# Kernel optimization log

Hardware: AMD Instinct MI355X
Metric: run time of the kernel (lower is better)

Reference implementation:

```python
import jax, jax.numpy as jnp
import numpy as np

N = 50000
E = 800000
D_IN = 64
D_OUT = 64
H = 8
R = 8  # num_relations; relation id R is reserved for self-loops
NEG_SLOPE = 0.2
EPS = 1e-10


def setup_inputs() -> dict:
    key = jax.random.key(0)
    ks = jax.random.split(key, 7)
    x = jax.random.normal(ks[0], (N, D_IN), jnp.float32)
    # xavier_uniform-like scale for W_tau, kaiming-like for query
    w_scale = (6.0 / (D_IN + D_OUT)) ** 0.5
    W_tau = jax.random.normal(ks[1], (R + 1, D_OUT, D_IN), jnp.float32) * w_scale
    query = jax.random.normal(ks[2], (R + 1, H, 2 * D_OUT // H), jnp.float32) * 0.1
    node_in = jax.random.randint(ks[3], (E,), 0, N, jnp.int32)
    node_out = jax.random.randint(ks[4], (E,), 0, N, jnp.int32)
    relation = jax.random.randint(ks[5], (E,), 0, R, jnp.int32)
    edge_weight = jax.random.uniform(ks[6], (E,), jnp.float32)
    return {"x": x, "W_tau": W_tau, "query": query, "node_in": node_in,
            "node_out": node_out, "relation": relation, "edge_weight": edge_weight}


def reference(x, W_tau, query, node_in, node_out, relation, edge_weight):
    n_node = x.shape[0]
    rp1, d_out, _ = W_tau.shape  # num_relations + 1
    n_head = query.shape[1]

    # append self-loop edges with relation id = num_relations, weight 1
    self_idx = jnp.arange(n_node, dtype=node_in.dtype)
    ni = jnp.concatenate([node_in, self_idx])            # [M]
    no = jnp.concatenate([node_out, self_idx])           # [M]
    rel = jnp.concatenate([relation, jnp.full((n_node,), rp1 - 1, dtype=relation.dtype)])
    ew = jnp.concatenate([edge_weight, jnp.ones((n_node,), edge_weight.dtype)])[:, None]  # [M,1]

    # per-relation linear transform of all nodes: [R+1, N, D_out]
    hidden = jnp.einsum('rdi,ni->rnd', W_tau, x)

    # gather endpoint features per edge (relation-specific)
    h_in = hidden[rel, ni]    # [M, D_out]
    h_out = hidden[rel, no]   # [M, D_out]
    m = h_in.shape[0]

    # interleaved stack then head split, matching torch stack(dim=-1).view
    key_feat = jnp.stack([h_in, h_out], axis=-1).reshape(m, n_head, -1)  # [M,H,2*D/H]
    w = jnp.einsum('mhd,mhd->mh', query[rel], key_feat)                  # [M,H]
    w = jax.nn.leaky_relu(w, NEG_SLOPE)

    # segment softmax (stabilized by per-node max), normalizer is scatter-MEAN (faithful)
    mx = jax.ops.segment_max(w, no, num_segments=n_node)[no]
    att = jnp.exp(w - mx) * ew                                           # [M,H]
    cnt = jax.ops.segment_sum(jnp.ones((m,), x.dtype), no, num_segments=n_node)  # [N]
    norm = (jax.ops.segment_sum(att, no, num_segments=n_node) / cnt[:, None])[no]
    att = att / (norm + EPS)

    value = h_in.reshape(m, n_head, d_out // n_head)                     # [M,H,D/H]
    msg = (att[..., None] * value).reshape(m, d_out)                     # [M,D_out]

    # aggregate: scatter-mean over destination nodes, then ReLU (combine)
    update = jax.ops.segment_sum(msg, no, num_segments=n_node) / cnt[:, None]
    return jax.nn.relu(update)
```

## Files before the change

### kernel.cpp

```cpp
#include <hip/hip_runtime.h>
#include <math.h>

#define N_NODES 50000
#define N_EDGES 800000
#define DOUT 64
#define NHEAD 8
#define RP1 9
#define NEG_SLOPE 0.2f
#define EPS_F 1e-10f
#define M_TOT (N_EDGES + N_NODES)
#define NW (RP1 * DOUT * DOUT)
#define RNG (N_NODES / 8)
#define EPB 2048
#define CHUNKS ((M_TOT + EPB - 1) / EPB)
#define BUCK 48
#define MBLK ((M_TOT + 255) / 256)
#define FILLB (CHUNKS * 8)
#define K1B ((N_NODES + 63) / 64)
#define K1PAD 784

typedef __attribute__((ext_vector_type(8))) short bf16x8;
typedef __attribute__((ext_vector_type(4))) float f32x4;

__device__ __forceinline__ unsigned short f2bf(float f) {
    unsigned int u = __float_as_uint(f);
    unsigned int r = (u + 0x7FFFu + ((u >> 16) & 1u)) >> 16;
    return (unsigned short)r;
}
__device__ __forceinline__ float bf2f(unsigned short s) {
    return __uint_as_float(((unsigned int)s) << 16);
}

__global__ __launch_bounds__(256) void kprep2(const int* __restrict__ node_in,
                                              const int* __restrict__ relation,
                                              const float* __restrict__ edge_weight,
                                              const float* __restrict__ W,
                                              int2* __restrict__ meta_by_m,
                                              unsigned short* __restrict__ Wb,
                                              int* __restrict__ cursor) {
    int m = blockIdx.x * 256 + threadIdx.x;
    if (m < NW / 4) {
        int i = m * 4;
        float4 v = *(const float4*)(W + i);
        ushort4 o; o.x = f2bf(v.x); o.y = f2bf(v.y); o.z = f2bf(v.z); o.w = f2bf(v.w);
        *(ushort4*)(Wb + i) = o;
    }
    if (m < N_NODES) cursor[m] = 0;
    if (m >= M_TOT) return;
    int ni, rl; float ew;
    if (m < N_EDGES) {
        ni = node_in[m]; rl = relation[m]; ew = edge_weight[m];
    } else {
        ni = m - N_EDGES; rl = RP1 - 1; ew = 1.0f;
    }
    int2 v; v.x = ni | (rl << 16); v.y = __float_as_int(ew);
    meta_by_m[m] = v;
}

__global__ __launch_bounds__(256) void kbig(const float* __restrict__ x,
                                            const unsigned short* __restrict__ Wb,
                                            unsigned short* __restrict__ hiddenb,
                                            const int* __restrict__ node_out,
                                            const int2* __restrict__ meta_by_m,
                                            int* __restrict__ cursor,
                                            int2* __restrict__ bucket) {
    const int t = threadIdx.x;

    if (blockIdx.x >= K1PAD) {
        const int f = blockIdx.x - K1PAD;
        const int r = f & 7;
        const int chunk = f >> 3;
        const int lo = r * RNG;
        const int hi = lo + RNG;
        int m = chunk * EPB + t;
#pragma unroll
        for (int it = 0; it < EPB / 256; it++, m += 256) {
            if (m < M_TOT) {
                int2 v = meta_by_m[m];
                int no = (m < N_EDGES) ? node_out[m] : (m - N_EDGES);
                if (no >= lo && no < hi) {
                    int pos = atomicAdd(&cursor[no], 1);
                    if (pos < BUCK) bucket[(size_t)no * BUCK + pos] = v;
                }
            }
        }
        return;
    }

    const int bx = blockIdx.x;
    if (bx >= K1B) return;
    __shared__ float xs[64 * 68];
    __shared__ unsigned short st[4 * 16 * 72];
    const int wv = t >> 6, lane = t & 63;
    const int quad = lane >> 4, l16 = lane & 15;
    const int base = bx * 64 + wv * 16;

    for (int q = t; q < 64 * 64 / 4; q += 256) {
        int flat = q * 4;
        int row = flat >> 6;
        int col = flat & 63;
        int n = bx * 64 + row;
        float4 v = make_float4(0.f, 0.f, 0.f, 0.f);
        if (n < N_NODES) v = *(const float4*)(x + (size_t)n * 64 + col);
        float* p = &xs[row * 68 + col];
        p[0] = v.x; p[1] = v.y; p[2] = v.z; p[3] = v.w;
    }
    __syncthreads();

    int arowl = wv * 16 + l16;
    bf16x8 a0, a1;
#pragma unroll
    for (int j = 0; j < 8; j++) {
        a0[j] = (short)f2bf(xs[arowl * 68 + quad * 8 + j]);
        a1[j] = (short)f2bf(xs[arowl * 68 + quad * 8 + 32 + j]);
    }

    unsigned short* sw = &st[wv * 16 * 72];

    for (int r = 0; r < RP1; r++) {
        const unsigned short* Wr = Wb + r * 4096;
        f32x4 acc[4];
#pragma unroll
        for (int dt = 0; dt < 4; dt++) {
            const bf16x8 b0 = *(const bf16x8*)(Wr + (dt * 16 + l16) * 64 + quad * 8);
            const bf16x8 b1 = *(const bf16x8*)(Wr + (dt * 16 + l16) * 64 + quad * 8 + 32);
            f32x4 c = {0.f, 0.f, 0.f, 0.f};
            c = __builtin_amdgcn_mfma_f32_16x16x32_bf16(a0, b0, c, 0, 0, 0);
            c = __builtin_amdgcn_mfma_f32_16x16x32_bf16(a1, b1, c, 0, 0, 0);
            acc[dt] = c;
        }
#pragma unroll
        for (int dt = 0; dt < 4; dt++) {
#pragma unroll
            for (int v = 0; v < 4; v++) {
                sw[(quad * 4 + v) * 72 + dt * 16 + l16] = f2bf(acc[dt][v]);
            }
        }
        __threadfence_block();
#pragma unroll
        for (int q = 0; q < 2; q++) {
            int cid = q * 64 + lane;
            int row = cid >> 3;
            int ch = cid & 7;
            int n = base + row;
            if (n < N_NODES) {
                bf16x8 v = *(const bf16x8*)(sw + row * 72 + ch * 8);
                *(bf16x8*)(hiddenb + ((size_t)r * N_NODES + n) * 64 + ch * 8) = v;
            }
        }
        __threadfence_block();
    }
}

__global__ __launch_bounds__(256) void k3_fused2(const unsigned short* __restrict__ hiddenb,
                                                 const float* __restrict__ query,
                                                 const int2* __restrict__ bucket,
                                                 const int* __restrict__ deg,
                                                 float* __restrict__ out) {
    __shared__ float qe[RP1 * 64];
    __shared__ float qo[RP1 * 64];
    __shared__ int2  meta[4][64];
    __shared__ float bho[4][2][72];

    const int t = threadIdx.x;
    for (int q = t; q < RP1 * 64; q += 256) {
        int j = q & 7, rh = q >> 3;
        qe[q] = query[rh * 16 + 2 * j];
        qo[q] = query[rh * 16 + 2 * j + 1];
    }
    __syncthreads();

    const int wv = t >> 6, lane = t & 63;
    const int pairi = blockIdx.x * 4 + wv;
    const int nA = pairi * 2, nB = nA + 1;
    const int e_lo = lane >> 3, h = lane & 7;

    {
        const int prel = lane >> 3, ph = lane & 7;
        bf16x8 ra = *(const bf16x8*)(hiddenb + ((size_t)(prel * N_NODES + nA)) * 64 + ph * 8);
        bf16x8 rb = *(const bf16x8*)(hiddenb + ((size_t)(prel * N_NODES + nB)) * 64 + ph * 8);
        bf16x8 r8 = ra;
        if (lane < 16) {
            int n8 = (lane < 8) ? nA : nB;
            r8 = *(const bf16x8*)(hiddenb + ((size_t)(8 * N_NODES + n8)) * 64 + (lane & 7) * 8);
        }
        const float* qop = &qo[(prel * 8 + ph) * 8];
        float da = 0.f, db = 0.f;
#pragma unroll
        for (int j = 0; j < 8; j++) {
            da += qop[j] * bf2f((unsigned short)ra[j]);
            db += qop[j] * bf2f((unsigned short)rb[j]);
        }
        bho[wv][0][prel * 8 + ph] = da;
        bho[wv][1][prel * 8 + ph] = db;
        if (lane < 16) {
            const float* q8p = &qo[(64 + (lane & 7)) * 8];
            float d8 = 0.f;
#pragma unroll
            for (int j = 0; j < 8; j++) d8 += q8p[j] * bf2f((unsigned short)r8[j]);
            bho[wv][(lane < 8) ? 0 : 1][64 + (lane & 7)] = d8;
        }
    }
    __threadfence_block();

    const int degAi = deg[nA], degBi = deg[nB];
    const int begA = nA * BUCK, endA = begA + min(degAi, BUCK);
    const int begB = nB * BUCK, endB = begB + min(degBi, BUCK);
    const float degA = (float)degAi, degB = (float)degBi;

    float accA[8] = {0.f, 0.f, 0.f, 0.f, 0.f, 0.f, 0.f, 0.f};
    float accB[8] = {0.f, 0.f, 0.f, 0.f, 0.f, 0.f, 0.f, 0.f};
    float spA = 0.f, spB = 0.f;
    int cbA = begA, cbB = begB;

    while (cbA < endA || cbB < endB) {
        const int cA = min(32, endA - cbA);
        const int cB = min(32, endB - cbB);

        int2 mt; mt.x = nA | ((RP1 - 1) << 16); mt.y = 0;
        if (lane < 32) {
            if (lane < cA) mt = bucket[cbA + lane];
        } else {
            int l2 = lane - 32;
            if (l2 < cB) mt = bucket[cbB + l2];
        }
        meta[wv][lane] = mt;
        __threadfence_block();

        const int npA = (cA + 7) >> 3, npB = (cB + 7) >> 3;

        bf16x8 rA[4], rB[4];
        int relA[4], relB[4]; float ewA[4], ewB[4];
#pragma unroll
        for (int p = 0; p < 4; p++) {
            if (p < npA) {
                int2 m2 = meta[wv][p * 8 + e_lo];
                int ni = m2.x & 0xffff, rl = m2.x >> 16;
                relA[p] = rl; ewA[p] = __int_as_float(m2.y);
                rA[p] = *(const bf16x8*)(hiddenb + ((size_t)(rl * N_NODES + ni)) * 64 + h * 8);
            }
            if (p < npB) {
                int2 m2 = meta[wv][32 + p * 8 + e_lo];
                int ni = m2.x & 0xffff, rl = m2.x >> 16;
                relB[p] = rl; ewB[p] = __int_as_float(m2.y);
                rB[p] = *(const bf16x8*)(hiddenb + ((size_t)(rl * N_NODES + ni)) * 64 + h * 8);
            }
        }

#pragma unroll
        for (int p = 0; p < 4; p++) {
            if (p < npA) {
                const float* qp = &qe[(relA[p] * 8 + h) * 8];
                float hif[8];
#pragma unroll
                for (int j = 0; j < 8; j++) hif[j] = bf2f((unsigned short)rA[p][j]);
                float wp = bho[wv][0][relA[p] * 8 + h];
#pragma unroll
                for (int j = 0; j < 8; j++) wp += qp[j] * hif[j];
                wp = (wp > 0.f) ? wp : NEG_SLOPE * wp;
                float pa = __expf(wp) * ewA[p];
#pragma unroll
                for (int j = 0; j < 8; j++) accA[j] += pa * hif[j];
                spA += pa;
            }
            if (p < npB) {
                const float* qp = &qe[(relB[p] * 8 + h) * 8];
                float hif[8];
#pragma unroll
                for (int j = 0; j < 8; j++) hif[j] = bf2f((unsigned short)rB[p][j]);
                float wp = bho[wv][1][relB[p] * 8 + h];
#pragma unroll
                for (int j = 0; j < 8; j++) wp += qp[j] * hif[j];
                wp = (wp > 0.f) ? wp : NEG_SLOPE * wp;
                float pa = __expf(wp) * ewB[p];
#pragma unroll
                for (int j = 0; j < 8; j++) accB[j] += pa * hif[j];
                spB += pa;
            }
        }

        cbA += cA; cbB += cB;
    }

#pragma unroll
    for (int j = 0; j < 8; j++) {
        accA[j] += __shfl_xor(accA[j], 8);
        accA[j] += __shfl_xor(accA[j], 16);
        accA[j] += __shfl_xor(accA[j], 32);
        accB[j] += __shfl_xor(accB[j], 8);
        accB[j] += __shfl_xor(accB[j], 16);
        accB[j] += __shfl_xor(accB[j], 32);
    }
    spA += __shfl_xor(spA, 8); spA += __shfl_xor(spA, 16); spA += __shfl_xor(spA, 32);
    spB += __shfl_xor(spB, 8); spB += __shfl_xor(spB, 16); spB += __shfl_xor(spB, 32);

    if (lane < 8) {
        const float s = 1.f / ((spA / degA + EPS_F) * degA);
        float4 o0, o1;
        o0.x = fmaxf(accA[0] * s, 0.f); o0.y = fmaxf(accA[1] * s, 0.f);
        o0.z = fmaxf(accA[2] * s, 0.f); o0.w = fmaxf(accA[3] * s, 0.f);
        o1.x = fmaxf(accA[4] * s, 0.f); o1.y = fmaxf(accA[5] * s, 0.f);
        o1.z = fmaxf(accA[6] * s, 0.f); o1.w = fmaxf(accA[7] * s, 0.f);
        float* op = out + (size_t)nA * 64 + lane * 8;
        *(float4*)(op) = o0; *(float4*)(op + 4) = o1;
    } else if (lane < 16) {
        const float s = 1.f / ((spB / degB + EPS_F) * degB);
        float4 o0, o1;
        o0.x = fmaxf(accB[0] * s, 0.f); o0.y = fmaxf(accB[1] * s, 0.f);
        o0.z = fmaxf(accB[2] * s, 0.f); o0.w = fmaxf(accB[3] * s, 0.f);
        o1.x = fmaxf(accB[4] * s, 0.f); o1.y = fmaxf(accB[5] * s, 0.f);
        o1.z = fmaxf(accB[6] * s, 0.f); o1.w = fmaxf(accB[7] * s, 0.f);
        float* op = out + (size_t)nB * 64 + (lane - 8) * 8;
        *(float4*)(op) = o0; *(float4*)(op + 4) = o1;
    }
}

extern "C" void kernel_launch(void* const* d_in, const int* in_sizes, int n_in,
                              void* d_out, int out_size, void* d_ws, size_t ws_size,
                              hipStream_t stream) {
    const float* x        = (const float*)d_in[0];
    const float* W_tau    = (const float*)d_in[1];
    const float* query    = (const float*)d_in[2];
    const int*   node_in  = (const int*)d_in[3];
    const int*   node_out = (const int*)d_in[4];
    const int*   relation = (const int*)d_in[5];
    const float* edge_w   = (const float*)d_in[6];
    float* out = (float*)d_out;

    char* ws = (char*)d_ws;
    unsigned short* hiddenb   = (unsigned short*)(ws);
    unsigned short* Wb        = (unsigned short*)(ws + 57600000);
    int2*           meta_by_m = (int2*)(ws + 57673728);
    int2*           bucket    = (int2*)(ws + 64473728);
    int*            cursor    = (int*)(ws + 83673728);

    kprep2<<<MBLK, 256, 0, stream>>>(node_in, relation, edge_w, W_tau,
                                     meta_by_m, Wb, cursor);

    kbig<<<K1PAD + FILLB, 256, 0, stream>>>(x, Wb, hiddenb, node_out, meta_by_m,
                                            cursor, bucket);

    k3_fused2<<<(N_NODES / 2 + 3) / 4, 256, 0, stream>>>(hiddenb, query, bucket,
                                                         cursor, out);
}
```

Before: 178.2 us.

## Load x directly to registers and hoist bucket/hidden loads before query staging

In the transform kernel, the shared-memory staging of x is removed; each lane loads its MFMA A-operand rows straight from global memory, which drops a barrier and the LDS traffic. In the aggregation kernel, the degree, bucket-metadata and self-feature loads are issued before the query table is staged into shared memory, so their latency overlaps that setup. The per-chunk while loop with its shared-memory meta buffer is replaced by a single 32-slot pass that distributes metadata with wave shuffles, plus a separate tail path for nodes with more than 32 edges. The tail path adds code size and some register pressure.

```diff
diff --git a/kernel.cpp b/kernel.cpp
--- a/kernel.cpp
+++ b/kernel.cpp
@@ -89,31 +89,27 @@
 
     const int bx = blockIdx.x;
     if (bx >= K1B) return;
-    __shared__ float xs[64 * 68];
     __shared__ unsigned short st[4 * 16 * 72];
     const int wv = t >> 6, lane = t & 63;
     const int quad = lane >> 4, l16 = lane & 15;
     const int base = bx * 64 + wv * 16;
 
-    for (int q = t; q < 64 * 64 / 4; q += 256) {
-        int flat = q * 4;
-        int row = flat >> 6;
-        int col = flat & 63;
-        int n = bx * 64 + row;
-        float4 v = make_float4(0.f, 0.f, 0.f, 0.f);
-        if (n < N_NODES) v = *(const float4*)(x + (size_t)n * 64 + col);
-        float* p = &xs[row * 68 + col];
-        p[0] = v.x; p[1] = v.y; p[2] = v.z; p[3] = v.w;
-    }
-    __syncthreads();
-
-    int arowl = wv * 16 + l16;
+    int arow = base + l16;
+    if (arow >= N_NODES) arow = N_NODES - 1;
+    const float* xr = x + (size_t)arow * 64 + quad * 8;
+    const float4 f0 = *(const float4*)(xr + 0);
+    const float4 f1 = *(const float4*)(xr + 4);
+    const float4 f2 = *(const float4*)(xr + 32);
+    const float4 f3 = *(const float4*)(xr + 36);
     bf16x8 a0, a1;
-#pragma unroll
-    for (int j = 0; j < 8; j++) {
-        a0[j] = (short)f2bf(xs[arowl * 68 + quad * 8 + j]);
-        a1[j] = (short)f2bf(xs[arowl * 68 + quad * 8 + 32 + j]);
-    }
+    a0[0] = (short)f2bf(f0.x); a0[1] = (short)f2bf(f0.y);
+    a0[2] = (short)f2bf(f0.z); a0[3] = (short)f2bf(f0.w);
+    a0[4] = (short)f2bf(f1.x); a0[5] = (short)f2bf(f1.y);
+    a0[6] = (short)f2bf(f1.z); a0[7] = (short)f2bf(f1.w);
+    a1[0] = (short)f2bf(f2.x); a1[1] = (short)f2bf(f2.y);
+    a1[2] = (short)f2bf(f2.z); a1[3] = (short)f2bf(f2.w);
+    a1[4] = (short)f2bf(f3.x); a1[5] = (short)f2bf(f3.y);
+    a1[6] = (short)f2bf(f3.z); a1[7] = (short)f2bf(f3.w);
 
     unsigned short* sw = &st[wv * 16 * 72];
 
@@ -159,10 +155,28 @@
                                                  float* __restrict__ out) {
     __shared__ float qe[RP1 * 64];
     __shared__ float qo[RP1 * 64];
-    __shared__ int2  meta[4][64];
     __shared__ float bho[4][2][72];
 
     const int t = threadIdx.x;
+    const int wv = t >> 6, lane = t & 63;
+    const int pairi = blockIdx.x * 4 + wv;
+    const int nA = pairi * 2, nB = nA + 1;
+    const int e_lo = lane >> 3, h = lane & 7;
+
+    const int degAi = deg[nA], degBi = deg[nB];
+    const int slot = lane & 31;
+    const int nn = (lane >= 32) ? nB : nA;
+    const int2 mt0 = bucket[(size_t)nn * BUCK + slot];
+
+    const int prel = lane >> 3, ph = lane & 7;
+    const bf16x8 ra = *(const bf16x8*)(hiddenb + ((size_t)(prel * N_NODES + nA)) * 64 + ph * 8);
+    const bf16x8 rb = *(const bf16x8*)(hiddenb + ((size_t)(prel * N_NODES + nB)) * 64 + ph * 8);
+    bf16x8 r8 = ra;
+    if (lane < 16) {
+        int n8 = (lane < 8) ? nA : nB;
+        r8 = *(const bf16x8*)(hiddenb + ((size_t)(8 * N_NODES + n8)) * 64 + (lane & 7) * 8);
+    }
+
     for (int q = t; q < RP1 * 64; q += 256) {
         int j = q & 7, rh = q >> 3;
         qe[q] = query[rh * 16 + 2 * j];
@@ -170,20 +184,7 @@
     }
     __syncthreads();
 
-    const int wv = t >> 6, lane = t & 63;
-    const int pairi = blockIdx.x * 4 + wv;
-    const int nA = pairi * 2, nB = nA + 1;
-    const int e_lo = lane >> 3, h = lane & 7;
-
     {
-        const int prel = lane >> 3, ph = lane & 7;
-        bf16x8 ra = *(const bf16x8*)(hiddenb + ((size_t)(prel * N_NODES + nA)) * 64 + ph * 8);
-        bf16x8 rb = *(const bf16x8*)(hiddenb + ((size_t)(prel * N_NODES + nB)) * 64 + ph * 8);
-        bf16x8 r8 = ra;
-        if (lane < 16) {
-            int n8 = (lane < 8) ? nA : nB;
-            r8 = *(const bf16x8*)(hiddenb + ((size_t)(8 * N_NODES + n8)) * 64 + (lane & 7) * 8);
-        }
         const float* qop = &qo[(prel * 8 + ph) * 8];
         float da = 0.f, db = 0.f;
 #pragma unroll
@@ -203,83 +204,112 @@
     }
     __threadfence_block();
 
-    const int degAi = deg[nA], degBi = deg[nB];
-    const int begA = nA * BUCK, endA = begA + min(degAi, BUCK);
-    const int begB = nB * BUCK, endB = begB + min(degBi, BUCK);
+    const int cA = min(32, degAi);
+    const int cB = min(32, degBi);
+    const int npA = (cA + 7) >> 3, npB = (cB + 7) >> 3;
     const float degA = (float)degAi, degB = (float)degBi;
 
     float accA[8] = {0.f, 0.f, 0.f, 0.f, 0.f, 0.f, 0.f, 0.f};
     float accB[8] = {0.f, 0.f, 0.f, 0.f, 0.f, 0.f, 0.f, 0.f};
     float spA = 0.f, spB = 0.f;
-    int cbA = begA, cbB = begB;
-
-    while (cbA < endA || cbB < endB) {
-        const int cA = min(32, endA - cbA);
-        const int cB = min(32, endB - cbB);
-
-        int2 mt; mt.x = nA | ((RP1 - 1) << 16); mt.y = 0;
-        if (lane < 32) {
-            if (lane < cA) mt = bucket[cbA + lane];
-        } else {
-            int l2 = lane - 32;
-            if (l2 < cB) mt = bucket[cbB + l2];
-        }
-        meta[wv][lane] = mt;
-        __threadfence_block();
-
-        const int npA = (cA + 7) >> 3, npB = (cB + 7) >> 3;
-
-        bf16x8 rA[4], rB[4];
-        int relA[4], relB[4]; float ewA[4], ewB[4];
-#pragma unroll
-        for (int p = 0; p < 4; p++) {
-            if (p < npA) {
-                int2 m2 = meta[wv][p * 8 + e_lo];
+
+    bf16x8 rA[4], rB[4];
+    int relA[4], relB[4]; float ewA[4], ewB[4];
+#pragma unroll
+    for (int p = 0; p < 4; p++) {
+        const int s = p * 8 + e_lo;
+        if (p < npA) {
+            int mx = __shfl(mt0.x, s);
+            int my = __shfl(mt0.y, s);
+            if (s >= cA) { mx = nA | ((RP1 - 1) << 16); my = 0; }
+            int ni = mx & 0xffff, rl = mx >> 16;
+            relA[p] = rl; ewA[p] = __int_as_float(my);
+            rA[p] = *(const bf16x8*)(hiddenb + ((size_t)(rl * N_NODES + ni)) * 64 + h * 8);
+        }
+        if (p < npB) {
+            int mx = __shfl(mt0.x, 32 + s);
+            int my = __shfl(mt0.y, 32 + s);
+            if (s >= cB) { mx = nB | ((RP1 - 1) << 16); my = 0; }
+            int ni = mx & 0xffff, rl = mx >> 16;
+            relB[p] = rl; ewB[p] = __int_as_float(my);
+            rB[p] = *(const bf16x8*)(hiddenb + ((size_t)(rl * N_NODES + ni)) * 64 + h * 8);
+        }
+    }
+
+#pragma unroll
+    for (int p = 0; p < 4; p++) {
+        if (p < npA) {
+            const float* qp = &qe[(relA[p] * 8 + h) * 8];
+            float hif[8];
+#pragma unroll
+            for (int j = 0; j < 8; j++) hif[j] = bf2f((unsigned short)rA[p][j]);
+            float wp = bho[wv][0][relA[p] * 8 + h];
+#pragma unroll
+            for (int j = 0; j < 8; j++) wp += qp[j] * hif[j];
+            wp = (wp > 0.f) ? wp : NEG_SLOPE * wp;
+            float pa = __expf(wp) * ewA[p];
+#pragma unroll
+            for (int j = 0; j < 8; j++) accA[j] += pa * hif[j];
+            spA += pa;
+        }
+        if (p < npB) {
+            const float* qp = &qe[(relB[p] * 8 + h) * 8];
+            float hif[8];
+#pragma unroll
+            for (int j = 0; j < 8; j++) hif[j] = bf2f((unsigned short)rB[p][j]);
+            float wp = bho[wv][1][relB[p] * 8 + h];
+#pragma unroll
+            for (int j = 0; j < 8; j++) wp += qp[j] * hif[j];
+            wp = (wp > 0.f) ? wp : NEG_SLOPE * wp;
+            float pa = __expf(wp) * ewB[p];
+#pragma unroll
+            for (int j = 0; j < 8; j++) accB[j] += pa * hif[j];
+            spB += pa;
+        }
+    }
+
+    if (degAi > 32 || degBi > 32) {
+        const int capA = min(degAi, BUCK), capB = min(degBi, BUCK);
+#pragma unroll
+        for (int p = 0; p < 2; p++) {
+            const int s = 32 + p * 8 + e_lo;
+            if (s < capA) {
+                int2 m2 = bucket[(size_t)nA * BUCK + s];
                 int ni = m2.x & 0xffff, rl = m2.x >> 16;
-                relA[p] = rl; ewA[p] = __int_as_float(m2.y);
-                rA[p] = *(const bf16x8*)(hiddenb + ((size_t)(rl * N_NODES + ni)) * 64 + h * 8);
-            }
-            if (p < npB) {
-                int2 m2 = meta[wv][32 + p * 8 + e_lo];
-                int ni = m2.x & 0xffff, rl = m2.x >> 16;
-                relB[p] = rl; ewB[p] = __int_as_float(m2.y);
-                rB[p] = *(const bf16x8*)(hiddenb + ((size_t)(rl * N_NODES + ni)) * 64 + h * 8);
-            }
-        }
-
-#pragma unroll
-        for (int p = 0; p < 4; p++) {
-            if (p < npA) {
-                const float* qp = &qe[(relA[p] * 8 + h) * 8];
+                float ew = __int_as_float(m2.y);
+                bf16x8 r = *(const bf16x8*)(hiddenb + ((size_t)(rl * N_NODES + ni)) * 64 + h * 8);
+                const float* qp = &qe[(rl * 8 + h) * 8];
                 float hif[8];
 #pragma unroll
-                for (int j = 0; j < 8; j++) hif[j] = bf2f((unsigned short)rA[p][j]);
-                float wp = bho[wv][0][relA[p] * 8 + h];
+                for (int j = 0; j < 8; j++) hif[j] = bf2f((unsigned short)r[j]);
+                float wp = bho[wv][0][rl * 8 + h];
 #pragma unroll
                 for (int j = 0; j < 8; j++) wp += qp[j] * hif[j];
                 wp = (wp > 0.f) ? wp : NEG_SLOPE * wp;
-                float pa = __expf(wp) * ewA[p];
+                float pa = __expf(wp) * ew;
 #pragma unroll
                 for (int j = 0; j < 8; j++) accA[j] += pa * hif[j];
                 spA += pa;
             }
-            if (p < npB) {
-                const float* qp = &qe[(relB[p] * 8 + h) * 8];
+            if (s < capB) {
+                int2 m2 = bucket[(size_t)nB * BUCK + s];
+                int ni = m2.x & 0xffff, rl = m2.x >> 16;
+                float ew = __int_as_float(m2.y);
+                bf16x8 r = *(const bf16x8*)(hiddenb + ((size_t)(rl * N_NODES + ni)) * 64 + h * 8);
+                const float* qp = &qe[(rl * 8 + h) * 8];
                 float hif[8];
 #pragma unroll
-                for (int j = 0; j < 8; j++) hif[j] = bf2f((unsigned short)rB[p][j]);
-                float wp = bho[wv][1][relB[p] * 8 + h];
+                for (int j = 0; j < 8; j++) hif[j] = bf2f((unsigned short)r[j]);
+                float wp = bho[wv][1][rl * 8 + h];
 #pragma unroll
                 for (int j = 0; j < 8; j++) wp += qp[j] * hif[j];
                 wp = (wp > 0.f) ? wp : NEG_SLOPE * wp;
-                float pa = __expf(wp) * ewB[p];
+                float pa = __expf(wp) * ew;
 #pragma unroll
                 for (int j = 0; j < 8; j++) accB[j] += pa * hif[j];
                 spB += pa;
             }
         }
-
-        cbA += cA; cbB += cB;
     }
 
 #pragma unroll
```

After: 169.2 us. -5.0%, faster.
